# Kernel optimization log

Measured on AMD Instinct MI355X. Metric: run time of the kernel, lower is better.

## Reference

```python
import jax, jax.numpy as jnp
import numpy as np

N_NODES = 100000
N_EDGES = 3200000
N_FEAT = 128
N_GRAPHS = 256


def setup_inputs() -> dict:
    key = jax.random.key(0)
    ks = jax.random.split(key, 12)
    x = jax.random.normal(ks[0], (N_NODES, N_FEAT), dtype=jnp.float32)
    edge_index = jax.random.randint(ks[1], (2, N_EDGES), 0, N_NODES, dtype=jnp.int64)
    edge_weight = jax.random.uniform(ks[2], (N_EDGES,), dtype=jnp.float32)
    batch = jnp.sort(jax.random.randint(ks[3], (N_NODES,), 0, N_GRAPHS, dtype=jnp.int64))
    def glorot(k, shape):
        lim = np.sqrt(6.0 / (shape[0] + shape[1]))
        return jax.random.uniform(k, shape, dtype=jnp.float32, minval=-lim, maxval=lim)
    W1 = glorot(ks[4], (N_FEAT, 64))
    b1 = jnp.zeros((64,), dtype=jnp.float32)
    W2 = glorot(ks[5], (64, 32))
    b2 = jnp.zeros((32,), dtype=jnp.float32)
    Wl1 = glorot(ks[6], (32, 16))
    bl1 = jnp.zeros((16,), dtype=jnp.float32)
    Wl2 = glorot(ks[7], (16, 1))
    bl2 = jnp.zeros((1,), dtype=jnp.float32)
    return {"x": x, "edge_index": edge_index, "edge_weight": edge_weight,
            "batch": batch, "W1": W1, "b1": b1, "W2": W2, "b2": b2,
            "Wl1": Wl1, "bl1": bl1, "Wl2": Wl2, "bl2": bl2}


def gcn_conv(x, row, col, ew, W, b, num_nodes):
    # x' = D^-1/2 (A + I) D^-1/2 (x W) + b, weights on edges, self-loop weight 1
    h = x @ W  # [N, out]
    deg = jax.ops.segment_sum(ew, col, num_segments=num_nodes) + 1.0  # self-loops add 1
    dinv = jnp.where(deg > 0, jax.lax.rsqrt(deg), 0.0)
    norm = dinv[row] * ew * dinv[col]  # [E]
    msg = h[row] * norm[:, None]  # edge-wise gather + scale
    agg = jax.ops.segment_sum(msg, col, num_segments=num_nodes)
    agg = agg + h * (dinv * dinv)[:, None]  # self-loop contribution
    return agg + b


def reference(x, edge_index, edge_weight, batch, W1, b1, W2, b2, Wl1, bl1, Wl2, bl2):
    row, col = edge_index[0], edge_index[1]
    h = jax.nn.relu(gcn_conv(x, row, col, edge_weight, W1, b1, N_NODES))
    # dropout is identity in eval mode
    h = gcn_conv(h, row, col, edge_weight, W2, b2, N_NODES)
    u = jax.ops.segment_sum(h, batch, num_segments=N_GRAPHS)  # global_add_pool
    out = jax.nn.relu(u @ Wl1 + bl1)
    out = out @ Wl2 + bl2
    return out.reshape(-1)
```

## Files before the change

kernel.cpp:

```cpp
#include <hip/hip_runtime.h>
#include <hip/hip_bf16.h>

#define N_NODES 100000
#define N_EDGES 3200000
#define N_GRAPHS 256

#define NBUCK 391
#define SORT_ITEMS 2048
#define NB_SORT ((N_EDGES + SORT_ITEMS - 1) / SORT_ITEMS)
#define HIST_N (NBUCK * NB_SORT)
#define ROW_MASK 131071

__device__ __forceinline__ float bfl(int d) {
    return __uint_as_float(((unsigned)d) << 16);
}
__device__ __forceinline__ float bfh(int d) {
    return __uint_as_float(((unsigned)d) & 0xffff0000u);
}
__device__ __forceinline__ unsigned short f2bf(float f) {
    __hip_bfloat16 b = __float2bfloat16(f);
    return *(unsigned short*)&b;
}

__global__ __launch_bounds__(256) void hist_kernel(const int* __restrict__ col,
                                                   int* __restrict__ hist) {
    __shared__ int h[NBUCK];
    int tid = threadIdx.x;
    for (int i = tid; i < NBUCK; i += 256) h[i] = 0;
    __syncthreads();
    int base = blockIdx.x * SORT_ITEMS + tid * 4;
    #pragma unroll
    for (int l = 0; l < SORT_ITEMS / 1024; ++l) {
        int e = base + l * 1024;
        if (e < N_EDGES) {
            int4 c4 = *(const int4*)&col[e];
            atomicAdd(&h[c4.x >> 8], 1);
            atomicAdd(&h[c4.y >> 8], 1);
            atomicAdd(&h[c4.z >> 8], 1);
            atomicAdd(&h[c4.w >> 8], 1);
        }
    }
    __syncthreads();
    for (int i = tid; i < NBUCK; i += 256) hist[i * NB_SORT + blockIdx.x] = h[i];
}

__global__ __launch_bounds__(256) void scanA_kernel(int* __restrict__ a,
                                                    int* __restrict__ bsum, int n) {
    __shared__ int s[256];
    int tid = threadIdx.x;
    int base = blockIdx.x * 4096 + tid * 16;
    int v[16];
    int sum = 0;
    #pragma unroll
    for (int i = 0; i < 16; ++i) { v[i] = (base + i < n) ? a[base + i] : 0; sum += v[i]; }
    s[tid] = sum;
    __syncthreads();
    for (int d = 1; d < 256; d <<= 1) {
        int x = (tid >= d) ? s[tid - d] : 0;
        __syncthreads();
        s[tid] += x;
        __syncthreads();
    }
    int run = s[tid] - sum;
    #pragma unroll
    for (int i = 0; i < 16; ++i) {
        if (base + i < n) a[base + i] = run;
        run += v[i];
    }
    if (tid == 255) bsum[blockIdx.x] = s[255];
}

__global__ __launch_bounds__(256) void scanB_kernel(int* bsum, int nb) {
    __shared__ int s[256];
    int tid = threadIdx.x;
    int v = (tid < nb) ? bsum[tid] : 0;
    s[tid] = v;
    __syncthreads();
    for (int d = 1; d < 256; d <<= 1) {
        int x = (tid >= d) ? s[tid - d] : 0;
        __syncthreads();
        s[tid] += x;
        __syncthreads();
    }
    if (tid < nb) bsum[tid] = s[tid] - v;
}

__global__ __launch_bounds__(256) void scanC_kernel(int* a, const int* __restrict__ bsum, int n) {
    int i = blockIdx.x * 256 + threadIdx.x;
    if (i < n) a[i] += bsum[i >> 12];
}

__global__ __launch_bounds__(256) void scatter_sort_kernel(const int* __restrict__ col,
                                                           const int* __restrict__ row,
                                                           const float* __restrict__ ew,
                                                           const int* __restrict__ hist,
                                                           int2* __restrict__ rw2) {
    __shared__ int offs[NBUCK];
    int tid = threadIdx.x;
    for (int i = tid; i < NBUCK; i += 256) offs[i] = hist[i * NB_SORT + blockIdx.x];
    __syncthreads();
    int base = blockIdx.x * SORT_ITEMS + tid * 4;
    #pragma unroll
    for (int l = 0; l < SORT_ITEMS / 1024; ++l) {
        int e = base + l * 1024;
        if (e < N_EDGES) {
            int4 c4 = *(const int4*)&col[e];
            int4 r4 = *(const int4*)&row[e];
            float4 w4 = *(const float4*)&ew[e];
            int p0 = atomicAdd(&offs[c4.x >> 8], 1);
            int p1 = atomicAdd(&offs[c4.y >> 8], 1);
            int p2 = atomicAdd(&offs[c4.z >> 8], 1);
            int p3 = atomicAdd(&offs[c4.w >> 8], 1);
            int2 v0; v0.x = r4.x | ((c4.x & 255) << 17); v0.y = __float_as_int(w4.x);
            int2 v1; v1.x = r4.y | ((c4.y & 255) << 17); v1.y = __float_as_int(w4.y);
            int2 v2; v2.x = r4.z | ((c4.z & 255) << 17); v2.y = __float_as_int(w4.z);
            int2 v3; v3.x = r4.w | ((c4.w & 255) << 17); v3.y = __float_as_int(w4.w);
            rw2[p0] = v0;
            rw2[p1] = v1;
            rw2[p2] = v2;
            rw2[p3] = v3;
        }
    }
}

__global__ __launch_bounds__(256) void build_kernel(const int* __restrict__ hist,
                                                    const int2* __restrict__ rw2,
                                                    int* __restrict__ off,
                                                    int* __restrict__ cnt,
                                                    float* __restrict__ dinv,
                                                    int2* __restrict__ csr) {
    int b = blockIdx.x;
    int tid = threadIdx.x;
    int begin = hist[b * NB_SORT];
    int end = (b + 1 < NBUCK) ? hist[(b + 1) * NB_SORT] : N_EDGES;
    __shared__ int lcnt[256];
    __shared__ float ldeg[256];
    __shared__ int s[256];
    __shared__ int curo[256];
    lcnt[tid] = 0;
    ldeg[tid] = 0.f;
    __syncthreads();
    for (int e = begin + tid; e < end; e += 512) {
        int2 a = rw2[e];
        int e2 = e + 256;
        int2 c = (e2 < end) ? rw2[e2] : make_int2(0, 0);
        atomicAdd(&lcnt[a.x >> 17], 1);
        atomicAdd(&ldeg[a.x >> 17], __int_as_float(a.y));
        if (e2 < end) {
            atomicAdd(&lcnt[c.x >> 17], 1);
            atomicAdd(&ldeg[c.x >> 17], __int_as_float(c.y));
        }
    }
    __syncthreads();
    int v = lcnt[tid];
    s[tid] = v;
    __syncthreads();
    for (int d = 1; d < 256; d <<= 1) {
        int x = (tid >= d) ? s[tid - d] : 0;
        __syncthreads();
        s[tid] += x;
        __syncthreads();
    }
    int excl = s[tid] - v;
    int node = (b << 8) + tid;
    if (node < N_NODES) {
        off[node] = begin + excl;
        cnt[node] = v;
        dinv[node] = rsqrtf(1.0f + ldeg[tid]);
    }
    curo[tid] = begin + excl;
    __syncthreads();
    for (int e = begin + tid; e < end; e += 512) {
        int2 a = rw2[e];
        int e2 = e + 256;
        int2 c = (e2 < end) ? rw2[e2] : make_int2(0, 0);
        int pa = atomicAdd(&curo[a.x >> 17], 1);
        csr[pa] = make_int2(a.x & ROW_MASK, a.y);
        if (e2 < end) {
            int pc = atomicAdd(&curo[c.x >> 17], 1);
            csr[pc] = make_int2(c.x & ROW_MASK, c.y);
        }
    }
}

template <int IN, int OUT, int ROWS>
__global__ __launch_bounds__(256) void gemm_bf16_kernel(const float* __restrict__ X,
                                                        const float* __restrict__ W,
                                                        const float* __restrict__ scale,
                                                        unsigned short* __restrict__ H, int n) {
    constexpr int BK = 16;
    constexpr int TX = OUT / 4;
    constexpr int TY = ROWS / 4;
    static_assert(TX * TY == 256, "block must be 256 threads");
    constexpr int XSS = ROWS + 4;
    constexpr int WSS = OUT + 4;
    __shared__ float xsT[BK][XSS];
    __shared__ float ws[BK][WSS];
    int tid = threadIdx.x;
    int tx = tid % TX, ty = tid / TX;
    int r0 = blockIdx.x * ROWS;
    float acc[4][4] = {};
    for (int k0 = 0; k0 < IN; k0 += BK) {
        constexpr int XL = (ROWS * BK) / (256 * 4);
        #pragma unroll
        for (int l = 0; l < XL; ++l) {
            int t = tid + l * 256;
            int rr = t >> 2;
            int kp = (t & 3) * 4;
            float4 v = make_float4(0.f, 0.f, 0.f, 0.f);
            int gr = r0 + rr;
            if (gr < n) v = *(const float4*)&X[(size_t)gr * IN + k0 + kp];
            xsT[kp + 0][rr] = v.x;
            xsT[kp + 1][rr] = v.y;
            xsT[kp + 2][rr] = v.z;
            xsT[kp + 3][rr] = v.w;
        }
        constexpr int WL = (BK * OUT) / 4;
        if (tid < WL) {
            int kr = tid / TX;
            int cp = (tid % TX) * 4;
            float4 v = *(const float4*)&W[(size_t)(k0 + kr) * OUT + cp];
            *(float4*)&ws[kr][cp] = v;
        }
        __syncthreads();
        #pragma unroll
        for (int kk = 0; kk < BK; ++kk) {
            float4 a = *(const float4*)&xsT[kk][ty * 4];
            float4 b = *(const float4*)&ws[kk][tx * 4];
            float av[4] = {a.x, a.y, a.z, a.w};
            float bv[4] = {b.x, b.y, b.z, b.w};
            #pragma unroll
            for (int i = 0; i < 4; ++i) {
                #pragma unroll
                for (int j = 0; j < 4; ++j) acc[i][j] = fmaf(av[i], bv[j], acc[i][j]);
            }
        }
        __syncthreads();
    }
    #pragma unroll
    for (int i = 0; i < 4; ++i) {
        int gr = r0 + ty * 4 + i;
        if (gr < n) {
            float sc = scale[gr];
            ushort4 o;
            o.x = f2bf(acc[i][0] * sc);
            o.y = f2bf(acc[i][1] * sc);
            o.z = f2bf(acc[i][2] * sc);
            o.w = f2bf(acc[i][3] * sc);
            *(ushort4*)&H[(size_t)gr * OUT + tx * 4] = o;
        }
    }
}

__global__ __launch_bounds__(256) void agg1_kernel(const int2* __restrict__ csr,
                                                   const int* __restrict__ off,
                                                   const int* __restrict__ cnt,
                                                   const float* __restrict__ dinv,
                                                   const unsigned short* __restrict__ h1t,
                                                   const float* __restrict__ b1,
                                                   float* __restrict__ h1p) {
    int lane = threadIdx.x & 63;
    int node = blockIdx.x * 4 + (threadIdx.x >> 6);
    int es = lane >> 3;
    int fb = lane & 7;
    int s = off[node], c = cnt[node];
    float acc[8] = {};
    for (int j0 = 0; j0 < c; j0 += 64) {
        int m = min(64, c - j0);
        int2 e = make_int2(0, 0);
        if (lane < m) e = csr[s + j0 + lane];
        int ng = (m + 7) >> 3;
        int g = 0;
        for (; g + 2 <= ng; g += 2) {
            int s0 = g * 8 + es;
            int s1 = s0 + 8;
            int r0 = __shfl(e.x, s0);
            float w0 = __int_as_float(__shfl(e.y, s0));
            int r1 = __shfl(e.x, s1);
            float w1 = __int_as_float(__shfl(e.y, s1));
            int4 d0 = *(const int4*)(h1t + (((size_t)r0) << 6) + (fb << 3));
            int4 d1 = *(const int4*)(h1t + (((size_t)r1) << 6) + (fb << 3));
            acc[0] = fmaf(w0, bfl(d0.x), acc[0]);
            acc[1] = fmaf(w0, bfh(d0.x), acc[1]);
            acc[2] = fmaf(w0, bfl(d0.y), acc[2]);
            acc[3] = fmaf(w0, bfh(d0.y), acc[3]);
            acc[4] = fmaf(w0, bfl(d0.z), acc[4]);
            acc[5] = fmaf(w0, bfh(d0.z), acc[5]);
            acc[6] = fmaf(w0, bfl(d0.w), acc[6]);
            acc[7] = fmaf(w0, bfh(d0.w), acc[7]);
            acc[0] = fmaf(w1, bfl(d1.x), acc[0]);
            acc[1] = fmaf(w1, bfh(d1.x), acc[1]);
            acc[2] = fmaf(w1, bfl(d1.y), acc[2]);
            acc[3] = fmaf(w1, bfh(d1.y), acc[3]);
            acc[4] = fmaf(w1, bfl(d1.z), acc[4]);
            acc[5] = fmaf(w1, bfh(d1.z), acc[5]);
            acc[6] = fmaf(w1, bfl(d1.w), acc[6]);
            acc[7] = fmaf(w1, bfh(d1.w), acc[7]);
        }
        if (g < ng) {
            int s0 = g * 8 + es;
            int r0 = __shfl(e.x, s0);
            float w0 = __int_as_float(__shfl(e.y, s0));
            int4 d0 = *(const int4*)(h1t + (((size_t)r0) << 6) + (fb << 3));
            acc[0] = fmaf(w0, bfl(d0.x), acc[0]);
            acc[1] = fmaf(w0, bfh(d0.x), acc[1]);
            acc[2] = fmaf(w0, bfl(d0.y), acc[2]);
            acc[3] = fmaf(w0, bfh(d0.y), acc[3]);
            acc[4] = fmaf(w0, bfl(d0.z), acc[4]);
            acc[5] = fmaf(w0, bfh(d0.z), acc[5]);
            acc[6] = fmaf(w0, bfl(d0.w), acc[6]);
            acc[7] = fmaf(w0, bfh(d0.w), acc[7]);
        }
    }
    #pragma unroll
    for (int mask = 8; mask <= 32; mask <<= 1) {
        #pragma unroll
        for (int k = 0; k < 8; ++k) acc[k] += __shfl_xor(acc[k], mask);
    }
    if (es == 0) {
        float di = dinv[node];
        int4 ds = *(const int4*)(h1t + (((size_t)node) << 6) + (fb << 3));
        float4 bv0 = *(const float4*)&b1[fb * 8];
        float4 bv1 = *(const float4*)&b1[fb * 8 + 4];
        float4 o0, o1;
        o0.x = fmaxf(fmaf(acc[0] + bfl(ds.x), di, bv0.x), 0.f);
        o0.y = fmaxf(fmaf(acc[1] + bfh(ds.x), di, bv0.y), 0.f);
        o0.z = fmaxf(fmaf(acc[2] + bfl(ds.y), di, bv0.z), 0.f);
        o0.w = fmaxf(fmaf(acc[3] + bfh(ds.y), di, bv0.w), 0.f);
        o1.x = fmaxf(fmaf(acc[4] + bfl(ds.z), di, bv1.x), 0.f);
        o1.y = fmaxf(fmaf(acc[5] + bfh(ds.z), di, bv1.y), 0.f);
        o1.z = fmaxf(fmaf(acc[6] + bfl(ds.w), di, bv1.z), 0.f);
        o1.w = fmaxf(fmaf(acc[7] + bfh(ds.w), di, bv1.w), 0.f);
        float* po = h1p + (size_t)node * 64 + fb * 8;
        *(float4*)po = o0;
        *(float4*)(po + 4) = o1;
    }
}

__global__ __launch_bounds__(256) void agg2_kernel(const int2* __restrict__ csr,
                                                   const int* __restrict__ off,
                                                   const int* __restrict__ cnt,
                                                   const float* __restrict__ dinv,
                                                   const unsigned short* __restrict__ h2t,
                                                   const float* __restrict__ b2,
                                                   float* __restrict__ h2p) {
    int lane = threadIdx.x & 63;
    int half = lane >> 5;
    int hl = lane & 31;
    int es = hl >> 2;
    int fb = hl & 3;
    int wid = threadIdx.x >> 6;
    int node = blockIdx.x * 8 + wid * 2 + half;
    int s = off[node], c = cnt[node];
    int lbase = half << 5;
    float acc[8] = {};
    for (int j0 = 0; j0 < c; j0 += 32) {
        int m = min(32, c - j0);
        int2 e = make_int2(0, 0);
        if (hl < m) e = csr[s + j0 + hl];
        int ng = (m + 7) >> 3;
        int g = 0;
        for (; g + 2 <= ng; g += 2) {
            int s0 = lbase + g * 8 + es;
            int s1 = s0 + 8;
            int r0 = __shfl(e.x, s0);
            float w0 = __int_as_float(__shfl(e.y, s0));
            int r1 = __shfl(e.x, s1);
            float w1 = __int_as_float(__shfl(e.y, s1));
            int4 d0 = *(const int4*)(h2t + (((size_t)r0) << 5) + (fb << 3));
            int4 d1 = *(const int4*)(h2t + (((size_t)r1) << 5) + (fb << 3));
            acc[0] = fmaf(w0, bfl(d0.x), acc[0]);
            acc[1] = fmaf(w0, bfh(d0.x), acc[1]);
            acc[2] = fmaf(w0, bfl(d0.y), acc[2]);
            acc[3] = fmaf(w0, bfh(d0.y), acc[3]);
            acc[4] = fmaf(w0, bfl(d0.z), acc[4]);
            acc[5] = fmaf(w0, bfh(d0.z), acc[5]);
            acc[6] = fmaf(w0, bfl(d0.w), acc[6]);
            acc[7] = fmaf(w0, bfh(d0.w), acc[7]);
            acc[0] = fmaf(w1, bfl(d1.x), acc[0]);
            acc[1] = fmaf(w1, bfh(d1.x), acc[1]);
            acc[2] = fmaf(w1, bfl(d1.y), acc[2]);
            acc[3] = fmaf(w1, bfh(d1.y), acc[3]);
            acc[4] = fmaf(w1, bfl(d1.z), acc[4]);
            acc[5] = fmaf(w1, bfh(d1.z), acc[5]);
            acc[6] = fmaf(w1, bfl(d1.w), acc[6]);
            acc[7] = fmaf(w1, bfh(d1.w), acc[7]);
        }
        if (g < ng) {
            int s0 = lbase + g * 8 + es;
            int r0 = __shfl(e.x, s0);
            float w0 = __int_as_float(__shfl(e.y, s0));
            int4 d0 = *(const int4*)(h2t + (((size_t)r0) << 5) + (fb << 3));
            acc[0] = fmaf(w0, bfl(d0.x), acc[0]);
            acc[1] = fmaf(w0, bfh(d0.x), acc[1]);
            acc[2] = fmaf(w0, bfl(d0.y), acc[2]);
            acc[3] = fmaf(w0, bfh(d0.y), acc[3]);
            acc[4] = fmaf(w0, bfl(d0.z), acc[4]);
            acc[5] = fmaf(w0, bfh(d0.z), acc[5]);
            acc[6] = fmaf(w0, bfl(d0.w), acc[6]);
            acc[7] = fmaf(w0, bfh(d0.w), acc[7]);
        }
    }
    #pragma unroll
    for (int mask = 4; mask <= 16; mask <<= 1) {
        #pragma unroll
        for (int k = 0; k < 8; ++k) acc[k] += __shfl_xor(acc[k], mask);
    }
    if (es == 0) {
        float di = dinv[node];
        int4 ds = *(const int4*)(h2t + (((size_t)node) << 5) + (fb << 3));
        float4 bv0 = *(const float4*)&b2[fb * 8];
        float4 bv1 = *(const float4*)&b2[fb * 8 + 4];
        float4 o0, o1;
        o0.x = fmaf(acc[0] + bfl(ds.x), di, bv0.x);
        o0.y = fmaf(acc[1] + bfh(ds.x), di, bv0.y);
        o0.z = fmaf(acc[2] + bfl(ds.y), di, bv0.z);
        o0.w = fmaf(acc[3] + bfh(ds.y), di, bv0.w);
        o1.x = fmaf(acc[4] + bfl(ds.z), di, bv1.x);
        o1.y = fmaf(acc[5] + bfh(ds.z), di, bv1.y);
        o1.z = fmaf(acc[6] + bfl(ds.w), di, bv1.z);
        o1.w = fmaf(acc[7] + bfh(ds.w), di, bv1.w);
        float* po = h2p + (size_t)node * 32 + fb * 8;
        *(float4*)po = o0;
        *(float4*)(po + 4) = o1;
    }
}

__global__ __launch_bounds__(256) void pool_kernel(const float* __restrict__ h2p,
                                                   const int* __restrict__ batch,
                                                   float* __restrict__ u) {
    int g = blockIdx.x;
    int lo = 0, hi = N_NODES;
    while (lo < hi) { int m = (lo + hi) >> 1; if (batch[m] < g) lo = m + 1; else hi = m; }
    int start = lo;
    hi = N_NODES;
    while (lo < hi) { int m = (lo + hi) >> 1; if (batch[m] < g + 1) lo = m + 1; else hi = m; }
    int end = lo;
    int f = threadIdx.x & 31, grp = threadIdx.x >> 5;
    float acc = 0.f;
    for (int n = start + grp; n < end; n += 8) acc += h2p[(size_t)n * 32 + f];
    __shared__ float red[8][32];
    red[grp][f] = acc;
    __syncthreads();
    if (threadIdx.x < 32) {
        float sum = 0.f;
        #pragma unroll
        for (int k = 0; k < 8; ++k) sum += red[k][threadIdx.x];
        u[g * 32 + threadIdx.x] = sum;
    }
}

__global__ __launch_bounds__(256) void head_kernel(const float* __restrict__ u,
                                                   const float* __restrict__ Wl1,
                                                   const float* __restrict__ bl1,
                                                   const float* __restrict__ Wl2,
                                                   const float* __restrict__ bl2,
                                                   float* __restrict__ out) {
    int g = threadIdx.x;
    float uu[32];
    #pragma unroll
    for (int k = 0; k < 32; ++k) uu[k] = u[g * 32 + k];
    float o = bl2[0];
    #pragma unroll
    for (int j = 0; j < 16; ++j) {
        float h = bl1[j];
        #pragma unroll
        for (int k = 0; k < 32; ++k) h = fmaf(uu[k], Wl1[k * 16 + j], h);
        o = fmaf(fmaxf(h, 0.f), Wl2[j], o);
    }
    out[g] = o;
}

extern "C" void kernel_launch(void* const* d_in, const int* in_sizes, int n_in,
                              void* d_out, int out_size, void* d_ws, size_t ws_size,
                              hipStream_t stream) {
    const float* x     = (const float*)d_in[0];
    const int*   ei    = (const int*)d_in[1];
    const float* ew    = (const float*)d_in[2];
    const int*   batch = (const int*)d_in[3];
    const float* W1    = (const float*)d_in[4];
    const float* b1    = (const float*)d_in[5];
    const float* W2    = (const float*)d_in[6];
    const float* b2    = (const float*)d_in[7];
    const float* Wl1   = (const float*)d_in[8];
    const float* bl1   = (const float*)d_in[9];
    const float* Wl2   = (const float*)d_in[10];
    const float* bl2   = (const float*)d_in[11];
    float* out = (float*)d_out;

    const int* row = ei;
    const int* col = ei + N_EDGES;

    char* p = (char*)d_ws;
    auto alloc = [&](size_t bytes) {
        char* q = p;
        p += (bytes + 255) & ~(size_t)255;
        return q;
    };
    int*   hist   = (int*)alloc((size_t)HIST_N * 4);
    int*   bsum   = (int*)alloc(1024 * 4);
    int2*  rw2    = (int2*)alloc((size_t)N_EDGES * 8);
    int*   off    = (int*)alloc(N_NODES * 4);
    int*   cnt    = (int*)alloc(N_NODES * 4);
    float* dinv   = (float*)alloc(N_NODES * 4);
    int2*  csr    = (int2*)alloc((size_t)N_EDGES * 8);
    unsigned short* h1t = (unsigned short*)rw2;
    float* h1p    = (float*)alloc((size_t)N_NODES * 64 * 4);
    unsigned short* h2t = (unsigned short*)alloc((size_t)N_NODES * 32 * 2);
    float* h2p    = (float*)alloc((size_t)N_NODES * 32 * 4);
    float* u      = (float*)alloc(N_GRAPHS * 32 * 4);

    const int nbScan = (HIST_N + 4095) / 4096;

    hist_kernel<<<NB_SORT, 256, 0, stream>>>(col, hist);
    scanA_kernel<<<nbScan, 256, 0, stream>>>(hist, bsum, HIST_N);
    scanB_kernel<<<1, 256, 0, stream>>>(bsum, nbScan);
    scanC_kernel<<<(HIST_N + 255) / 256, 256, 0, stream>>>(hist, bsum, HIST_N);
    scatter_sort_kernel<<<NB_SORT, 256, 0, stream>>>(col, row, ew, hist, rw2);
    build_kernel<<<NBUCK, 256, 0, stream>>>(hist, rw2, off, cnt, dinv, csr);

    gemm_bf16_kernel<128, 64, 64><<<(N_NODES + 63) / 64, 256, 0, stream>>>(x, W1, dinv, h1t, N_NODES);
    agg1_kernel<<<N_NODES / 4, 256, 0, stream>>>(csr, off, cnt, dinv, h1t, b1, h1p);
    gemm_bf16_kernel<64, 32, 128><<<(N_NODES + 127) / 128, 256, 0, stream>>>(h1p, W2, dinv, h2t, N_NODES);
    agg2_kernel<<<N_NODES / 8, 256, 0, stream>>>(csr, off, cnt, dinv, h2t, b2, h2p);
    pool_kernel<<<N_GRAPHS, 256, 0, stream>>>(h2p, batch, u);
    head_kernel<<<1, 256, 0, stream>>>(u, Wl1, bl1, Wl2, bl2, out);
}
```

Measured before the change: 257.1 us.

## Enlarge GEMM row tiles, unroll CSR build loops, and double sort chunk size

The GEMM kernel now computes 8 rows by 4 columns per thread, doubling the rows per block, so each shared-memory weight load is reused across more rows. The build kernel's edge loops are unrolled to four loads per iteration to raise memory-level parallelism. SORT_ITEMS is doubled, which halves the number of sort blocks and the histogram size, at the cost of more work per block (assuming the hidden sort kernels scale correctly with it). The larger accumulator arrays raise register pressure and may lower occupancy.

Result: no change. 256.1 us (-0.4%).

```diff
diff --git a/kernel.cpp b/kernel.cpp
--- a/kernel.cpp
+++ b/kernel.cpp
@@ -6,7 +6,7 @@
 #define N_GRAPHS 256
 
 #define NBUCK 391
-#define SORT_ITEMS 2048
+#define SORT_ITEMS 4096
 #define NB_SORT ((N_EDGES + SORT_ITEMS - 1) / SORT_ITEMS)
 #define HIST_N (NBUCK * NB_SORT)
 #define ROW_MASK 131071
@@ -140,16 +140,17 @@
     lcnt[tid] = 0;
     ldeg[tid] = 0.f;
     __syncthreads();
-    for (int e = begin + tid; e < end; e += 512) {
-        int2 a = rw2[e];
-        int e2 = e + 256;
-        int2 c = (e2 < end) ? rw2[e2] : make_int2(0, 0);
-        atomicAdd(&lcnt[a.x >> 17], 1);
-        atomicAdd(&ldeg[a.x >> 17], __int_as_float(a.y));
-        if (e2 < end) {
-            atomicAdd(&lcnt[c.x >> 17], 1);
-            atomicAdd(&ldeg[c.x >> 17], __int_as_float(c.y));
-        }
+    for (int e = begin + tid; e < end; e += 1024) {
+        int2 a0 = rw2[e];
+        int e1 = e + 256, e2 = e + 512, e3 = e + 768;
+        int2 a1 = (e1 < end) ? rw2[e1] : make_int2(0, 0);
+        int2 a2 = (e2 < end) ? rw2[e2] : make_int2(0, 0);
+        int2 a3 = (e3 < end) ? rw2[e3] : make_int2(0, 0);
+        atomicAdd(&lcnt[a0.x >> 17], 1);
+        atomicAdd(&ldeg[a0.x >> 17], __int_as_float(a0.y));
+        if (e1 < end) { atomicAdd(&lcnt[a1.x >> 17], 1); atomicAdd(&ldeg[a1.x >> 17], __int_as_float(a1.y)); }
+        if (e2 < end) { atomicAdd(&lcnt[a2.x >> 17], 1); atomicAdd(&ldeg[a2.x >> 17], __int_as_float(a2.y)); }
+        if (e3 < end) { atomicAdd(&lcnt[a3.x >> 17], 1); atomicAdd(&ldeg[a3.x >> 17], __int_as_float(a3.y)); }
     }
     __syncthreads();
     int v = lcnt[tid];
@@ -170,16 +171,17 @@
     }
     curo[tid] = begin + excl;
     __syncthreads();
-    for (int e = begin + tid; e < end; e += 512) {
-        int2 a = rw2[e];
-        int e2 = e + 256;
-        int2 c = (e2 < end) ? rw2[e2] : make_int2(0, 0);
-        int pa = atomicAdd(&curo[a.x >> 17], 1);
-        csr[pa] = make_int2(a.x & ROW_MASK, a.y);
-        if (e2 < end) {
-            int pc = atomicAdd(&curo[c.x >> 17], 1);
-            csr[pc] = make_int2(c.x & ROW_MASK, c.y);
-        }
+    for (int e = begin + tid; e < end; e += 1024) {
+        int2 a0 = rw2[e];
+        int e1 = e + 256, e2 = e + 512, e3 = e + 768;
+        int2 a1 = (e1 < end) ? rw2[e1] : make_int2(0, 0);
+        int2 a2 = (e2 < end) ? rw2[e2] : make_int2(0, 0);
+        int2 a3 = (e3 < end) ? rw2[e3] : make_int2(0, 0);
+        int p0 = atomicAdd(&curo[a0.x >> 17], 1);
+        csr[p0] = make_int2(a0.x & ROW_MASK, a0.y);
+        if (e1 < end) { int p = atomicAdd(&curo[a1.x >> 17], 1); csr[p] = make_int2(a1.x & ROW_MASK, a1.y); }
+        if (e2 < end) { int p = atomicAdd(&curo[a2.x >> 17], 1); csr[p] = make_int2(a2.x & ROW_MASK, a2.y); }
+        if (e3 < end) { int p = atomicAdd(&curo[a3.x >> 17], 1); csr[p] = make_int2(a3.x & ROW_MASK, a3.y); }
     }
 }
 
@@ -190,16 +192,14 @@
                                                         unsigned short* __restrict__ H, int n) {
     constexpr int BK = 16;
     constexpr int TX = OUT / 4;
-    constexpr int TY = ROWS / 4;
+    constexpr int TY = ROWS / 8;
     static_assert(TX * TY == 256, "block must be 256 threads");
-    constexpr int XSS = ROWS + 4;
-    constexpr int WSS = OUT + 4;
-    __shared__ float xsT[BK][XSS];
-    __shared__ float ws[BK][WSS];
+    __shared__ float xsT[BK][ROWS + 4];
+    __shared__ float ws[BK][OUT + 4];
     int tid = threadIdx.x;
     int tx = tid % TX, ty = tid / TX;
     int r0 = blockIdx.x * ROWS;
-    float acc[4][4] = {};
+    float acc[8][4] = {};
     for (int k0 = 0; k0 < IN; k0 += BK) {
         constexpr int XL = (ROWS * BK) / (256 * 4);
         #pragma unroll
@@ -216,7 +216,7 @@
             xsT[kp + 3][rr] = v.w;
         }
         constexpr int WL = (BK * OUT) / 4;
-        if (tid < WL) {
+        if (WL == 256 || tid < WL) {
             int kr = tid / TX;
             int cp = (tid % TX) * 4;
             float4 v = *(const float4*)&W[(size_t)(k0 + kr) * OUT + cp];
@@ -225,12 +225,13 @@
         __syncthreads();
         #pragma unroll
         for (int kk = 0; kk < BK; ++kk) {
-            float4 a = *(const float4*)&xsT[kk][ty * 4];
+            float4 a0 = *(const float4*)&xsT[kk][ty * 8];
+            float4 a1 = *(const float4*)&xsT[kk][ty * 8 + 4];
             float4 b = *(const float4*)&ws[kk][tx * 4];
-            float av[4] = {a.x, a.y, a.z, a.w};
+            float av[8] = {a0.x, a0.y, a0.z, a0.w, a1.x, a1.y, a1.z, a1.w};
             float bv[4] = {b.x, b.y, b.z, b.w};
             #pragma unroll
-            for (int i = 0; i < 4; ++i) {
+            for (int i = 0; i < 8; ++i) {
                 #pragma unroll
                 for (int j = 0; j < 4; ++j) acc[i][j] = fmaf(av[i], bv[j], acc[i][j]);
             }
@@ -238,8 +239,8 @@
         __syncthreads();
     }
     #pragma unroll
-    for (int i = 0; i < 4; ++i) {
-        int gr = r0 + ty * 4 + i;
+    for (int i = 0; i < 8; ++i) {
+        int gr = r0 + ty * 8 + i;
         if (gr < n) {
             float sc = scale[gr];
             ushort4 o;
@@ -519,9 +520,9 @@
     scatter_sort_kernel<<<NB_SORT, 256, 0, stream>>>(col, row, ew, hist, rw2);
     build_kernel<<<NBUCK, 256, 0, stream>>>(hist, rw2, off, cnt, dinv, csr);
 
-    gemm_bf16_kernel<128, 64, 64><<<(N_NODES + 63) / 64, 256, 0, stream>>>(x, W1, dinv, h1t, N_NODES);
+    gemm_bf16_kernel<128, 64, 128><<<(N_NODES + 127) / 128, 256, 0, stream>>>(x, W1, dinv, h1t, N_NODES);
     agg1_kernel<<<N_NODES / 4, 256, 0, stream>>>(csr, off, cnt, dinv, h1t, b1, h1p);
-    gemm_bf16_kernel<64, 32, 128><<<(N_NODES + 127) / 128, 256, 0, stream>>>(h1p, W2, dinv, h2t, N_NODES);
+    gemm_bf16_kernel<64, 32, 256><<<(N_NODES + 255) / 256, 256, 0, stream>>>(h1p, W2, dinv, h2t, N_NODES);
     agg2_kernel<<<N_NODES / 8, 256, 0, stream>>>(csr, off, cnt, dinv, h2t, b2, h2p);
     pool_kernel<<<N_GRAPHS, 256, 0, stream>>>(h2p, batch, u);
     head_kernel<<<1, 256, 0, stream>>>(u, Wl1, bl1, Wl2, bl2, out);
```
